# Kernel tuning notes

Measured on AMD Instinct MI355X. Metric: run time of the kernel, lower is better.

## Reference

```python
import jax, jax.numpy as jnp
import numpy as np

B, L, D, UNITS = 512, 64, 1024, 512

def setup_inputs() -> dict:
    key = jax.random.key(0)
    ks = jax.random.split(key, 8)
    sc = lambda n: 1.0 / np.sqrt(n)
    return {
        "features": jax.random.normal(ks[0], (B, L, D), jnp.float32),
        "hidden": jax.random.normal(ks[1], (B, UNITS), jnp.float32),
        "W1_w": jax.random.normal(ks[2], (D, UNITS), jnp.float32) * sc(D),
        "W1_b": jnp.zeros((UNITS,), jnp.float32),
        "W2_w": jax.random.normal(ks[3], (UNITS, UNITS), jnp.float32) * sc(UNITS),
        "W2_b": jnp.zeros((UNITS,), jnp.float32),
        "V_w": jax.random.normal(ks[4], (UNITS, 1), jnp.float32) * sc(UNITS),
        "V_b": jnp.zeros((1,), jnp.float32),
    }

def reference(features, hidden, W1_w, W1_b, W2_w, W2_b, V_w, V_b):
    # features: [B, L, D], hidden: [B, U]
    h = hidden @ W2_w + W2_b                      # [B, U]
    score = jnp.tanh(features @ W1_w + W1_b + h[:, None, :])  # [B, L, U]
    logits = score @ V_w + V_b                    # [B, L, 1]
    attn = jax.nn.softmax(logits, axis=1)         # softmax over L
    context = jnp.sum(attn * features, axis=1)    # [B, D]
    return context, attn
```

## Files before the change

kernel.cpp:

```cpp
#include <hip/hip_runtime.h>
#include <hip/hip_bf16.h>

#define Bb 512
#define Ll 64
#define Dd 1024
#define Uu 512

typedef __attribute__((ext_vector_type(8))) short short8;
typedef __attribute__((ext_vector_type(4))) float f32x4;
typedef __attribute__((ext_vector_type(4))) unsigned short u16x4;

__device__ __forceinline__ unsigned short f2bf(float x) {
  unsigned int u = __float_as_uint(x);
  u += 0x7FFF + ((u >> 16) & 1);
  return (unsigned short)(u >> 16);
}

__device__ __forceinline__ void gld16(const void* g, void* l) {
  auto gp = reinterpret_cast<const __attribute__((address_space(1))) unsigned int*>(
      reinterpret_cast<uintptr_t>(g));
  auto lp = reinterpret_cast<__attribute__((address_space(3))) unsigned int*>(
      reinterpret_cast<uintptr_t>(l));
  __builtin_amdgcn_global_load_lds(gp, lp, 16, 0, 0);
}

__global__ void __launch_bounds__(512) k_prep(const float* __restrict__ hidden,
                                              const float* __restrict__ W2w,
                                              const float* __restrict__ W2b,
                                              const float* __restrict__ W1w,
                                              float* __restrict__ h,
                                              unsigned char* __restrict__ W1s) {
  const int t = threadIdx.x;
  if (blockIdx.x < 128) {
    __shared__ float hid[4][Uu];
    const int b0 = blockIdx.x * 4;
#pragma unroll
    for (int i = 0; i < 4; ++i) hid[i][t] = hidden[(size_t)(b0 + i) * Uu + t];
    __syncthreads();
    float a0 = 0.f, a1 = 0.f, a2 = 0.f, a3 = 0.f;
    for (int k0 = 0; k0 < Uu; k0 += 8) {
      float wv[8];
#pragma unroll
      for (int j = 0; j < 8; ++j) wv[j] = W2w[(size_t)(k0 + j) * Uu + t];
#pragma unroll
      for (int j = 0; j < 8; ++j) {
        a0 += hid[0][k0 + j] * wv[j];
        a1 += hid[1][k0 + j] * wv[j];
        a2 += hid[2][k0 + j] * wv[j];
        a3 += hid[3][k0 + j] * wv[j];
      }
    }
    const float bb = W2b[t];
    h[(size_t)(b0 + 0) * Uu + t] = a0 + bb;
    h[(size_t)(b0 + 1) * Uu + t] = a1 + bb;
    h[(size_t)(b0 + 2) * Uu + t] = a2 + bb;
    h[(size_t)(b0 + 3) * Uu + t] = a3 + bb;
  } else {
    const int id = blockIdx.x - 128;
    const int kb = id >> 3;
    const int ub = id & 7;
    __shared__ float tile[32][68];
    {
      const int r = t >> 4;
      const int c4 = t & 15;
      const float4 v = *reinterpret_cast<const float4*>(
          &W1w[(size_t)(kb * 32 + r) * Uu + ub * 64 + c4 * 4]);
      *reinterpret_cast<float4*>(&tile[r][c4 * 4]) = v;
    }
    __syncthreads();
    if (t < 256) {
      const int ul = t >> 2;
      const int ch = t & 3;
      const int u = ub * 64 + ul;
      unsigned int px[4];
#pragma unroll
      for (int q = 0; q < 4; ++q) {
        const unsigned int lo = f2bf(tile[ch * 8 + q * 2][ul]);
        const unsigned int hi = f2bf(tile[ch * 8 + q * 2 + 1][ul]);
        px[q] = lo | (hi << 16);
      }
      const int sw = ch ^ (u & 3);
      uint4 pack;
      pack.x = px[0]; pack.y = px[1]; pack.z = px[2]; pack.w = px[3];
      *reinterpret_cast<uint4*>(&W1s[(size_t)kb * 32768 + u * 64 + sw * 16]) = pack;
    }
  }
}

__global__ void __launch_bounds__(1024) k_fused(
    const float* __restrict__ features,
    const unsigned char* __restrict__ W1s,
    const float* __restrict__ W1b,
    const float* __restrict__ h,
    const float* __restrict__ Vw,
    const float* __restrict__ Vb,
    float* __restrict__ out_ctx,
    float* __restrict__ out_attn) {
  __shared__ __align__(16) unsigned char smem[81920];
  unsigned char* bufA = smem;
  unsigned char* bufB = smem + 16384;

  const int b0 = blockIdx.x * 2;
  const int tid = threadIdx.x;
  const int lane = tid & 63;
  const int w = tid >> 6;
  const int wr = w >> 3;
  const int wc = w & 7;
  const int l15 = lane & 15;
  const int lg = lane >> 4;

  const float* featB = features + (size_t)b0 * Ll * Dd;

  const int ar = tid >> 3;
  const int ap = tid & 7;
  const float* ag = featB + (size_t)ar * Dd + ap * 4;
  const int awoff = ar * 64 + (((ap >> 1) ^ (ar & 3)) << 4) + (ap & 1) * 8;

  const int swl = (lg ^ (l15 & 3)) << 4;
  const int aoff0 = (wr * 64 + l15) * 64 + swl;
  const int boff0 = (wc * 64 + l15) * 64 + swl;

  f32x4 acc[4][4];
#pragma unroll
  for (int mi = 0; mi < 4; ++mi)
#pragma unroll
    for (int ni = 0; ni < 4; ++ni) acc[mi][ni] = (f32x4){0.f, 0.f, 0.f, 0.f};

  {
    const float4 va = *reinterpret_cast<const float4*>(ag);
    const unsigned char* src = W1s + (size_t)(w * 2) * 1024 + lane * 16;
    unsigned char* dst = bufB + (w * 2) * 1024;
    gld16(src, dst);
    gld16(src + 1024, dst + 1024);
    u16x4 pa = {f2bf(va.x), f2bf(va.y), f2bf(va.z), f2bf(va.w)};
    *reinterpret_cast<u16x4*>(bufA + awoff) = pa;
  }
  __syncthreads();

  for (int kt = 0; kt < 32; ++kt) {
    const int cur = kt & 1;
    const unsigned char* cA = bufA + cur * 8192;
    const unsigned char* cB = bufB + cur * 32768;
    float4 va;
    if (kt < 31) {
      va = *reinterpret_cast<const float4*>(ag + (kt + 1) * 32);
      const unsigned char* src = W1s + (size_t)(kt + 1) * 32768 + (w * 2) * 1024 + lane * 16;
      unsigned char* dst = bufB + (cur ^ 1) * 32768 + (w * 2) * 1024;
      gld16(src, dst);
      gld16(src + 1024, dst + 1024);
    }
    short8 afr[4], bfr[4];
#pragma unroll
    for (int mi = 0; mi < 4; ++mi)
      afr[mi] = *reinterpret_cast<const short8*>(cA + aoff0 + mi * 1024);
#pragma unroll
    for (int ni = 0; ni < 4; ++ni)
      bfr[ni] = *reinterpret_cast<const short8*>(cB + boff0 + ni * 1024);
#pragma unroll
    for (int mi = 0; mi < 4; ++mi)
#pragma unroll
      for (int ni = 0; ni < 4; ++ni)
        acc[mi][ni] = __builtin_amdgcn_mfma_f32_16x16x32_bf16(afr[mi], bfr[ni], acc[mi][ni], 0, 0, 0);
    if (kt < 31) {
      u16x4 pa = {f2bf(va.x), f2bf(va.y), f2bf(va.z), f2bf(va.w)};
      *reinterpret_cast<u16x4*>(bufA + (cur ^ 1) * 8192 + awoff) = pa;
    }
    __syncthreads();
  }

  float part[4][4];
#pragma unroll
  for (int mi = 0; mi < 4; ++mi)
#pragma unroll
    for (int r = 0; r < 4; ++r) part[mi][r] = 0.f;

  const int bt = b0 + wr;
#pragma unroll
  for (int ni = 0; ni < 4; ++ni) {
    const int col = wc * 64 + ni * 16 + l15;
    const float hb = h[(size_t)bt * Uu + col];
    const float b1 = W1b[col];
    const float vw = Vw[col];
#pragma unroll
    for (int mi = 0; mi < 4; ++mi)
#pragma unroll
      for (int r = 0; r < 4; ++r) {
        const float x = acc[mi][ni][r] + b1 + hb;
        const float e = __expf(2.f * x);
        part[mi][r] += vw * (1.f - 2.f / (e + 1.f));
      }
  }
  float* lpart = (float*)smem;
  float* attn_s = (float*)(smem + 4096);
#pragma unroll
  for (int mi = 0; mi < 4; ++mi)
#pragma unroll
    for (int r = 0; r < 4; ++r) {
      float v = part[mi][r];
      v += __shfl_xor(v, 1);
      v += __shfl_xor(v, 2);
      v += __shfl_xor(v, 4);
      v += __shfl_xor(v, 8);
      if (l15 == 0) lpart[(wr * 64 + mi * 16 + lg * 4 + r) * 8 + wc] = v;
    }
  __syncthreads();

  if (tid < 128) {
    const int bi = tid >> 6;
    const int row = tid & 63;
    float lgv = Vb[0];
#pragma unroll
    for (int j = 0; j < 8; ++j) lgv += lpart[(bi * 64 + row) * 8 + j];
    float m = lgv;
#pragma unroll
    for (int off = 32; off > 0; off >>= 1) m = fmaxf(m, __shfl_xor(m, off));
    const float e = __expf(lgv - m);
    float s = e;
#pragma unroll
    for (int off = 32; off > 0; off >>= 1) s += __shfl_xor(s, off);
    const float a = e / s;
    attn_s[tid] = a;
    out_attn[(size_t)(b0 + bi) * 64 + row] = a;
  }
  __syncthreads();

  {
    const int bi = tid >> 9;
    const int dq = tid & 511;
    const float* fb = features + (size_t)(b0 + bi) * Ll * Dd + dq * 2;
    float2 c2 = {0.f, 0.f};
#pragma unroll 8
    for (int l = 0; l < 64; ++l) {
      const float a = attn_s[bi * 64 + l];
      const float2 f = *reinterpret_cast<const float2*>(fb + (size_t)l * Dd);
      c2.x += a * f.x;
      c2.y += a * f.y;
    }
    *reinterpret_cast<float2*>(&out_ctx[(size_t)(b0 + bi) * Dd + dq * 2]) = c2;
  }
}

extern "C" void kernel_launch(void* const* d_in, const int* in_sizes, int n_in,
                              void* d_out, int out_size, void* d_ws, size_t ws_size,
                              hipStream_t stream) {
  const float* features = (const float*)d_in[0];
  const float* hidden   = (const float*)d_in[1];
  const float* W1w      = (const float*)d_in[2];
  const float* W1b      = (const float*)d_in[3];
  const float* W2w      = (const float*)d_in[4];
  const float* W2b      = (const float*)d_in[5];
  const float* Vw       = (const float*)d_in[6];
  const float* Vb       = (const float*)d_in[7];
  float* out_ctx  = (float*)d_out;
  float* out_attn = (float*)d_out + (size_t)Bb * Dd;

  float* h = (float*)d_ws;
  unsigned char* W1s = (unsigned char*)d_ws + (1u << 20);

  k_prep<<<384, 512, 0, stream>>>(hidden, W2w, W2b, W1w, h, W1s);
  k_fused<<<256, 1024, 0, stream>>>(features, W1s, W1b, h, Vw, Vb, out_ctx, out_attn);
}
```

Baseline: 285.5 us.

## Split context reduction out of fused attention kernel into separate kernel

Moves the attention-weighted sum over features from the tail of the fused GEMM/softmax kernel into a new standalone kernel with one block per batch and float4 loads. The fused kernel now only writes attention weights to global memory, which the new kernel reads back. This aims to avoid the serialized low-parallelism tail inside the large 1024-thread blocks and improve memory-level parallelism. In exchange it adds a kernel launch and re-reads all features from memory/cache instead of while the block's slice may be resident.

```diff
diff --git a/kernel.cpp b/kernel.cpp
--- a/kernel.cpp
+++ b/kernel.cpp
@@ -94,7 +94,6 @@
     const float* __restrict__ h,
     const float* __restrict__ Vw,
     const float* __restrict__ Vb,
-    float* __restrict__ out_ctx,
     float* __restrict__ out_attn) {
   __shared__ __align__(16) unsigned char smem[81920];
   unsigned char* bufA = smem;
@@ -191,7 +190,6 @@
       }
   }
   float* lpart = (float*)smem;
-  float* attn_s = (float*)(smem + 4096);
 #pragma unroll
   for (int mi = 0; mi < 4; ++mi)
 #pragma unroll
@@ -218,26 +216,30 @@
     float s = e;
 #pragma unroll
     for (int off = 32; off > 0; off >>= 1) s += __shfl_xor(s, off);
-    const float a = e / s;
-    attn_s[tid] = a;
-    out_attn[(size_t)(b0 + bi) * 64 + row] = a;
-  }
+    out_attn[(size_t)(b0 + bi) * 64 + row] = e / s;
+  }
+}
+
+__global__ void __launch_bounds__(256) k_ctx(const float* __restrict__ features,
+                                             const float* __restrict__ attn,
+                                             float* __restrict__ out_ctx) {
+  __shared__ float a_s[64];
+  const int b = blockIdx.x;
+  const int t = threadIdx.x;
+  if (t < 64) a_s[t] = attn[(size_t)b * 64 + t];
   __syncthreads();
-
-  {
-    const int bi = tid >> 9;
-    const int dq = tid & 511;
-    const float* fb = features + (size_t)(b0 + bi) * Ll * Dd + dq * 2;
-    float2 c2 = {0.f, 0.f};
+  const float* fb = features + (size_t)b * Ll * Dd + t * 4;
+  float4 acc = {0.f, 0.f, 0.f, 0.f};
 #pragma unroll 8
-    for (int l = 0; l < 64; ++l) {
-      const float a = attn_s[bi * 64 + l];
-      const float2 f = *reinterpret_cast<const float2*>(fb + (size_t)l * Dd);
-      c2.x += a * f.x;
-      c2.y += a * f.y;
-    }
-    *reinterpret_cast<float2*>(&out_ctx[(size_t)(b0 + bi) * Dd + dq * 2]) = c2;
-  }
+  for (int l = 0; l < 64; ++l) {
+    const float4 f = *reinterpret_cast<const float4*>(fb + (size_t)l * Dd);
+    const float a = a_s[l];
+    acc.x += a * f.x;
+    acc.y += a * f.y;
+    acc.z += a * f.z;
+    acc.w += a * f.w;
+  }
+  *reinterpret_cast<float4*>(out_ctx + (size_t)b * Dd + t * 4) = acc;
 }
 
 extern "C" void kernel_launch(void* const* d_in, const int* in_sizes, int n_in,
@@ -258,5 +260,6 @@
   unsigned char* W1s = (unsigned char*)d_ws + (1u << 20);
 
   k_prep<<<384, 512, 0, stream>>>(hidden, W2w, W2b, W1w, h, W1s);
-  k_fused<<<256, 1024, 0, stream>>>(features, W1s, W1b, h, Vw, Vb, out_ctx, out_attn);
-}
+  k_fused<<<256, 1024, 0, stream>>>(features, W1s, W1b, h, Vw, Vb, out_attn);
+  k_ctx<<<Bb, 256, 0, stream>>>(features, out_attn, out_ctx);
+}
```

After: 289.3 us. About the same (+1.3%).

## Load W1 fragments directly from global memory instead of staging through LDS

Applied to the files above, without the earlier changes.

Stores W1 in the prep kernel as a transposed bf16 [U][D] matrix. The fused kernel now reads B fragments straight from global memory (L2-cached) into registers, so the LDS double buffer for W1 and the async global-to-LDS copies are gone. Only the features tile stays in LDS, now with a 64-wide K step and an 8-way XOR swizzle, and the K loop is halved to 16 iterations of two MFMA sub-steps. This shrinks LDS use and halves the barriers, but it exposes global-load latency on the B operand with no software prefetch.

```diff
diff --git a/kernel.cpp b/kernel.cpp
--- a/kernel.cpp
+++ b/kernel.cpp
@@ -14,14 +14,6 @@
   unsigned int u = __float_as_uint(x);
   u += 0x7FFF + ((u >> 16) & 1);
   return (unsigned short)(u >> 16);
-}
-
-__device__ __forceinline__ void gld16(const void* g, void* l) {
-  auto gp = reinterpret_cast<const __attribute__((address_space(1))) unsigned int*>(
-      reinterpret_cast<uintptr_t>(g));
-  auto lp = reinterpret_cast<__attribute__((address_space(3))) unsigned int*>(
-      reinterpret_cast<uintptr_t>(l));
-  __builtin_amdgcn_global_load_lds(gp, lp, 16, 0, 0);
 }
 
 __global__ void __launch_bounds__(512) k_prep(const float* __restrict__ hidden,
@@ -29,7 +21,7 @@
                                               const float* __restrict__ W2b,
                                               const float* __restrict__ W1w,
                                               float* __restrict__ h,
-                                              unsigned char* __restrict__ W1s) {
+                                              unsigned short* __restrict__ W1T) {
   const int t = threadIdx.x;
   if (blockIdx.x < 128) {
     __shared__ float hid[4][Uu];
@@ -68,37 +60,27 @@
       *reinterpret_cast<float4*>(&tile[r][c4 * 4]) = v;
     }
     __syncthreads();
-    if (t < 256) {
-      const int ul = t >> 2;
-      const int ch = t & 3;
-      const int u = ub * 64 + ul;
-      unsigned int px[4];
-#pragma unroll
-      for (int q = 0; q < 4; ++q) {
-        const unsigned int lo = f2bf(tile[ch * 8 + q * 2][ul]);
-        const unsigned int hi = f2bf(tile[ch * 8 + q * 2 + 1][ul]);
-        px[q] = lo | (hi << 16);
-      }
-      const int sw = ch ^ (u & 3);
-      uint4 pack;
-      pack.x = px[0]; pack.y = px[1]; pack.z = px[2]; pack.w = px[3];
-      *reinterpret_cast<uint4*>(&W1s[(size_t)kb * 32768 + u * 64 + sw * 16]) = pack;
+    {
+      const int ul = t >> 3;
+      const int ch = t & 7;
+      u16x4 p;
+#pragma unroll
+      for (int q = 0; q < 4; ++q) p[q] = f2bf(tile[ch * 4 + q][ul]);
+      *reinterpret_cast<u16x4*>(&W1T[(size_t)(ub * 64 + ul) * Dd + kb * 32 + ch * 4]) = p;
     }
   }
 }
 
 __global__ void __launch_bounds__(1024) k_fused(
     const float* __restrict__ features,
-    const unsigned char* __restrict__ W1s,
+    const unsigned short* __restrict__ W1T,
     const float* __restrict__ W1b,
     const float* __restrict__ h,
     const float* __restrict__ Vw,
     const float* __restrict__ Vb,
     float* __restrict__ out_ctx,
     float* __restrict__ out_attn) {
-  __shared__ __align__(16) unsigned char smem[81920];
-  unsigned char* bufA = smem;
-  unsigned char* bufB = smem + 16384;
+  __shared__ __align__(16) unsigned char smem[32768];
 
   const int b0 = blockIdx.x * 2;
   const int tid = threadIdx.x;
@@ -107,18 +89,20 @@
   const int wr = w >> 3;
   const int wc = w & 7;
   const int l15 = lane & 15;
-  const int lg = lane >> 4;
+  const int lg = (lane >> 4) & 3;
 
   const float* featB = features + (size_t)b0 * Ll * Dd;
 
   const int ar = tid >> 3;
-  const int ap = tid & 7;
-  const float* ag = featB + (size_t)ar * Dd + ap * 4;
-  const int awoff = ar * 64 + (((ap >> 1) ^ (ar & 3)) << 4) + (ap & 1) * 8;
-
-  const int swl = (lg ^ (l15 & 3)) << 4;
-  const int aoff0 = (wr * 64 + l15) * 64 + swl;
-  const int boff0 = (wc * 64 + l15) * 64 + swl;
+  const int ch8 = tid & 7;
+  const float* ag = featB + (size_t)ar * Dd + ch8 * 8;
+  const int awoff = ar * 128 + ((ch8 ^ (ar & 7)) << 4);
+
+  const int e7 = l15 & 7;
+  const int sw0 = ((lg ^ e7) << 4);
+  const int arow = (wr * 64 + l15) * 128;
+
+  const unsigned short* bbase = W1T + (size_t)(wc * 64 + l15) * Dd + lg * 8;
 
   f32x4 acc[4][4];
 #pragma unroll
@@ -127,43 +111,44 @@
     for (int ni = 0; ni < 4; ++ni) acc[mi][ni] = (f32x4){0.f, 0.f, 0.f, 0.f};
 
   {
-    const float4 va = *reinterpret_cast<const float4*>(ag);
-    const unsigned char* src = W1s + (size_t)(w * 2) * 1024 + lane * 16;
-    unsigned char* dst = bufB + (w * 2) * 1024;
-    gld16(src, dst);
-    gld16(src + 1024, dst + 1024);
-    u16x4 pa = {f2bf(va.x), f2bf(va.y), f2bf(va.z), f2bf(va.w)};
-    *reinterpret_cast<u16x4*>(bufA + awoff) = pa;
+    const float4 v0 = *reinterpret_cast<const float4*>(ag);
+    const float4 v1 = *reinterpret_cast<const float4*>(ag + 4);
+    short8 pa;
+    pa[0] = f2bf(v0.x); pa[1] = f2bf(v0.y); pa[2] = f2bf(v0.z); pa[3] = f2bf(v0.w);
+    pa[4] = f2bf(v1.x); pa[5] = f2bf(v1.y); pa[6] = f2bf(v1.z); pa[7] = f2bf(v1.w);
+    *reinterpret_cast<short8*>(smem + awoff) = pa;
   }
   __syncthreads();
 
-  for (int kt = 0; kt < 32; ++kt) {
-    const int cur = kt & 1;
-    const unsigned char* cA = bufA + cur * 8192;
-    const unsigned char* cB = bufB + cur * 32768;
-    float4 va;
-    if (kt < 31) {
-      va = *reinterpret_cast<const float4*>(ag + (kt + 1) * 32);
-      const unsigned char* src = W1s + (size_t)(kt + 1) * 32768 + (w * 2) * 1024 + lane * 16;
-      unsigned char* dst = bufB + (cur ^ 1) * 32768 + (w * 2) * 1024;
-      gld16(src, dst);
-      gld16(src + 1024, dst + 1024);
-    }
-    short8 afr[4], bfr[4];
-#pragma unroll
-    for (int mi = 0; mi < 4; ++mi)
-      afr[mi] = *reinterpret_cast<const short8*>(cA + aoff0 + mi * 1024);
-#pragma unroll
-    for (int ni = 0; ni < 4; ++ni)
-      bfr[ni] = *reinterpret_cast<const short8*>(cB + boff0 + ni * 1024);
-#pragma unroll
-    for (int mi = 0; mi < 4; ++mi)
+  for (int kt = 0; kt < 16; ++kt) {
+    const unsigned char* cA = smem + (kt & 1) * 16384;
+    unsigned char* nA = smem + ((kt + 1) & 1) * 16384;
+    float4 v0, v1;
+    if (kt < 15) {
+      v0 = *reinterpret_cast<const float4*>(ag + (kt + 1) * 64);
+      v1 = *reinterpret_cast<const float4*>(ag + (kt + 1) * 64 + 4);
+    }
+#pragma unroll
+    for (int kk = 0; kk < 2; ++kk) {
+      const int sw = kk ? (sw0 ^ 64) : sw0;
+      short8 afr[4], bfr[4];
+#pragma unroll
+      for (int mi = 0; mi < 4; ++mi)
+        afr[mi] = *reinterpret_cast<const short8*>(cA + arow + mi * 2048 + sw);
 #pragma unroll
       for (int ni = 0; ni < 4; ++ni)
-        acc[mi][ni] = __builtin_amdgcn_mfma_f32_16x16x32_bf16(afr[mi], bfr[ni], acc[mi][ni], 0, 0, 0);
-    if (kt < 31) {
-      u16x4 pa = {f2bf(va.x), f2bf(va.y), f2bf(va.z), f2bf(va.w)};
-      *reinterpret_cast<u16x4*>(bufA + (cur ^ 1) * 8192 + awoff) = pa;
+        bfr[ni] = *reinterpret_cast<const short8*>(bbase + (size_t)ni * 16 * Dd + kt * 64 + kk * 32);
+#pragma unroll
+      for (int mi = 0; mi < 4; ++mi)
+#pragma unroll
+        for (int ni = 0; ni < 4; ++ni)
+          acc[mi][ni] = __builtin_amdgcn_mfma_f32_16x16x32_bf16(afr[mi], bfr[ni], acc[mi][ni], 0, 0, 0);
+    }
+    if (kt < 15) {
+      short8 pa;
+      pa[0] = f2bf(v0.x); pa[1] = f2bf(v0.y); pa[2] = f2bf(v0.z); pa[3] = f2bf(v0.w);
+      pa[4] = f2bf(v1.x); pa[5] = f2bf(v1.y); pa[6] = f2bf(v1.z); pa[7] = f2bf(v1.w);
+      *reinterpret_cast<short8*>(nA + awoff) = pa;
     }
     __syncthreads();
   }
@@ -186,8 +171,8 @@
 #pragma unroll
       for (int r = 0; r < 4; ++r) {
         const float x = acc[mi][ni][r] + b1 + hb;
-        const float e = __expf(2.f * x);
-        part[mi][r] += vw * (1.f - 2.f / (e + 1.f));
+        const float ex = __expf(2.f * x);
+        part[mi][r] += vw * (1.f - 2.f / (ex + 1.f));
       }
   }
   float* lpart = (float*)smem;
@@ -214,11 +199,11 @@
     float m = lgv;
 #pragma unroll
     for (int off = 32; off > 0; off >>= 1) m = fmaxf(m, __shfl_xor(m, off));
-    const float e = __expf(lgv - m);
-    float s = e;
+    const float ex = __expf(lgv - m);
+    float s = ex;
 #pragma unroll
     for (int off = 32; off > 0; off >>= 1) s += __shfl_xor(s, off);
-    const float a = e / s;
+    const float a = ex / s;
     attn_s[tid] = a;
     out_attn[(size_t)(b0 + bi) * 64 + row] = a;
   }
@@ -255,8 +240,8 @@
   float* out_attn = (float*)d_out + (size_t)Bb * Dd;
 
   float* h = (float*)d_ws;
-  unsigned char* W1s = (unsigned char*)d_ws + (1u << 20);
-
-  k_prep<<<384, 512, 0, stream>>>(hidden, W2w, W2b, W1w, h, W1s);
-  k_fused<<<256, 1024, 0, stream>>>(features, W1s, W1b, h, Vw, Vb, out_ctx, out_attn);
-}
+  unsigned short* W1T = (unsigned short*)((char*)d_ws + (1u << 20));
+
+  k_prep<<<384, 512, 0, stream>>>(hidden, W2w, W2b, W1w, h, W1T);
+  k_fused<<<256, 1024, 0, stream>>>(features, W1T, W1b, h, Vw, Vb, out_ctx, out_attn);
+}
```

Measured after the change: 316.3 us. +10.8%, slower.
